# Kernel optimization log

Hardware: AMD Instinct MI355X
Metric: run time of the kernel (lower is better)

The kernel has to match this reference:

```python
import jax, jax.numpy as jnp
import numpy as np

IN_FEATS = 128
OUT_FEATS = 128
ASSIGN_DIM = 256
BATCH_SIZE = 8
N = 12288
E = 196608
CPG = ASSIGN_DIM // BATCH_SIZE  # clusters per graph (block width of the mask)


def setup_inputs() -> dict:
    key = jax.random.key(0)
    ks = jax.random.split(key, 6)
    x = jax.random.normal(ks[0], (N, IN_FEATS), dtype=jnp.float32)
    edge_index = jax.random.randint(ks[1], (2, E), 0, N, dtype=jnp.int32)
    batch = jnp.sort(jax.random.randint(ks[2], (N,), 0, BATCH_SIZE, dtype=jnp.int32))
    s = 1.0 / np.sqrt(2 * IN_FEATS)
    W_embd = jax.random.uniform(ks[3], (2 * IN_FEATS, OUT_FEATS), minval=-s, maxval=s, dtype=jnp.float32)
    b_embd = jnp.zeros((OUT_FEATS,), jnp.float32)
    W_pool = jax.random.uniform(ks[4], (2 * IN_FEATS, ASSIGN_DIM), minval=-s, maxval=s, dtype=jnp.float32)
    b_pool = jnp.zeros((ASSIGN_DIM,), jnp.float32)
    return dict(x=x, edge_index=edge_index, batch=batch,
                W_embd=W_embd, b_embd=b_embd, W_pool=W_pool, b_pool=b_pool)


def _sage_conv(x, src, dst, W, b):
    # GraphSAGE mean aggregator, concat([self, agg]) @ W + b, row L2-normalize.
    agg = jax.ops.segment_sum(x[src], dst, num_segments=N)                 # [N, F]
    deg = jax.ops.segment_sum(jnp.ones((E,), x.dtype), dst, num_segments=N)
    agg = agg / jnp.maximum(deg, 1.0)[:, None]
    h = jnp.concatenate([x, agg], axis=-1) @ W + b
    return h / jnp.maximum(jnp.linalg.norm(h, axis=-1, keepdims=True), 1e-12)


def _masked_softmax_nonme(m, mask):
    # memory_efficient=False branch of masked_softmax
    r = jax.nn.softmax(m * mask, axis=-1)
    r = r * mask
    return r / (r.sum(axis=-1, keepdims=True) + 1e-13)


def reference(x, edge_index, batch, W_embd, b_embd, W_pool, b_pool):
    src, dst = edge_index[0], edge_index[1]
    embed = _sage_conv(x, src, dst, W_embd, b_embd)    # [N, out_feats]
    pooled = _sage_conv(x, src, dst, W_pool, b_pool)   # [N, assign_dim]

    # block-diagonal mask: node i sees the assign columns of its own graph
    col_graph = jnp.arange(ASSIGN_DIM, dtype=batch.dtype) // CPG
    mask = (batch[:, None] == col_graph[None, :]).astype(pooled.dtype)  # [N, assign_dim]

    result = _masked_softmax_nonme(pooled, mask)        # [N, assign_dim]
    h = result.T @ embed                                # [assign_dim, out_feats]

    # adjacency coarsening: S^T A S with edge weights = 1 (duplicates sum)
    Ar = jax.ops.segment_sum(result[dst], src, num_segments=N)  # A @ result
    adj_new = result.T @ Ar                              # [assign_dim, assign_dim]

    # link prediction loss: ||A_dense - S S^T||_F / N^2 (dense NxN, as original)
    A_dense = jnp.zeros((N, N), result.dtype).at[src, dst].add(1.0)
    adj_loss = jnp.linalg.norm(A_dense - result @ result.T) / (N ** 2)

    # entropy loss over Categorical(probs=mask): uniform over each block
    p = mask / mask.sum(axis=-1, keepdims=True)
    ent = -jnp.sum(jnp.where(p > 0, p * jnp.log(jnp.where(p > 0, p, 1.0)), 0.0), axis=-1)
    entropy_loss = ent.sum()

    return adj_new, h, adj_loss, entropy_loss
```

## Files before the change

### kernel.cpp

```cpp
#include <hip/hip_runtime.h>
#include <math.h>

#define NN 12288
#define EE 196608
#define FIN 128
#define AD 256
#define NG 8
#define ACH 32
#define GCH 16
#define BCAP 128
#define APITCH 8256
#define HPITCH 4160
#define GPITCH 1088

using short8 = __attribute__((ext_vector_type(8))) short;
using floatx4 = __attribute__((ext_vector_type(4))) float;

__device__ __forceinline__ unsigned short f2bf(float f) {
  union { float f; unsigned u; } v; v.f = f;
  unsigned r = v.u + 0x7FFFu + ((v.u >> 16) & 1u);
  return (unsigned short)(r >> 16);
}


__global__ __launch_bounds__(256) void k_setup(const float* __restrict__ We, const float* __restrict__ be,
    const float* __restrict__ Wp, const float* __restrict__ bp, const int* __restrict__ batch,
    unsigned* cnt_dst, unsigned* cnt_src, double* acc, unsigned* done,
    unsigned short* __restrict__ WTb, float* __restrict__ bcat, int* __restrict__ gstart) {
  unsigned i = blockIdx.x * 256u + threadIdx.x;
  if (i < 384u * 256u) {
    unsigned n = i >> 8, k = i & 255u;
    float v = (n < 128u) ? We[k * 128u + n] : Wp[k * 256u + (n - 128u)];
    WTb[i] = f2bf(v);
  }
  if (i < 384u) bcat[i] = (i < 128u) ? be[i] : bp[i - 128u];
  if (i < NN) { cnt_dst[i] = 0u; cnt_src[i] = 0u; }
  if (i < 3u) acc[i] = 0.0;
  if (i == 3u) *done = 0u;
  if (i <= NG) {
    int g = (int)i, lo = 0, hi = NN;
    while (lo < hi) { int mid = (lo + hi) >> 1; if (batch[mid] < g) lo = mid + 1; else hi = mid; }
    gstart[g] = lo;
  }
}


__global__ __launch_bounds__(256) void k_edgeB(const int* __restrict__ src, const int* __restrict__ dst,
    const int* __restrict__ batch,
    unsigned* cnt_dst, unsigned* cnt_src, int* __restrict__ bdst, int* __restrict__ bsrc) {
  unsigned e = blockIdx.x * 256u + threadIdx.x;
  if (e >= EE) return;
  int s = src[e], d = dst[e];
  unsigned p = atomicAdd(&cnt_dst[d], 1u);
  if (p < BCAP) bdst[(size_t)d * BCAP + p] = s;
  int gd = batch[d];
  unsigned q = atomicAdd(&cnt_src[s], 1u);
  if (q < BCAP) bsrc[(size_t)s * BCAP + q] = (gd << 14) | d;
}


__global__ __launch_bounds__(256) void k_dupagg(const float* __restrict__ x,
    const unsigned* __restrict__ cnt_dst, const int* __restrict__ bdst,
    unsigned short* __restrict__ Zb, unsigned* __restrict__ dup_part) {
  int node = blockIdx.x * 4 + (threadIdx.x >> 6);
  int lane = threadIdx.x & 63;
  unsigned deg = cnt_dst[node];
  unsigned m = deg < BCAP ? deg : BCAP;
  const int* bk = bdst + (size_t)node * BCAP;
  unsigned cnt = 0;
  for (unsigned i0 = 0; i0 < m; i0 += 64) {
    int si = (i0 + lane < m) ? bk[i0 + lane] : -1;
    for (unsigned j = 0; j < m; j++) {
      int sj = bk[j];
      cnt += (si == sj) ? 1u : 0u;
    }
  }
#pragma unroll
  for (int o = 32; o >= 1; o >>= 1) cnt += __shfl_xor(cnt, o, 64);
  if (lane == 0) dup_part[node] = cnt;
  const float2* x2 = (const float2*)x;
  float ax = 0.f, ay = 0.f;
  for (unsigned k = 0; k < m; k++) {
    int s = bk[k];
    float2 v = x2[(size_t)s * 64 + lane];
    ax += v.x; ay += v.y;
  }
  float inv = 1.f / fmaxf((float)deg, 1.f);
  float2 sv = x2[(size_t)node * 64 + lane];
  ushort2* Zb2 = (ushort2*)Zb;
  ushort2 a; a.x = f2bf(sv.x); a.y = f2bf(sv.y);
  ushort2 mm; mm.x = f2bf(ax * inv); mm.y = f2bf(ay * inv);
  Zb2[(size_t)node * 128 + lane] = a;
  Zb2[(size_t)node * 128 + 64 + lane] = mm;
}


__global__ __launch_bounds__(256) void k_gemmnorm(const unsigned short* __restrict__ Zb,
    const unsigned short* __restrict__ WTb, const float* __restrict__ bcat,
    const int* __restrict__ batch, float* __restrict__ embed, float* __restrict__ Rc) {
  __shared__ unsigned short Bl[24 * 512];
  __shared__ unsigned short Al[4 * 512];
  int t = threadIdx.x;
  int gm = blockIdx.x * 64;
  int w = t >> 6, l = t & 63;

  floatx4 acc[24] = {};

  for (int kc = 0; kc < 8; kc++) {
    __syncthreads();
#pragma unroll
    for (int i = 0; i < 7; i++) {
      int p = t + i * 256;
      if (p < 1536) {
        int n = p >> 2, quad = p & 3;
        uint4 v = *(const uint4*)&WTb[(size_t)n * 256 + kc * 32 + quad * 8];
        *(uint4*)&Bl[(n >> 4) * 512 + ((n & 15) + 16 * quad) * 8] = v;
      } else {
        int p2 = p - 1536;
        int m = p2 >> 2, quad = p2 & 3;
        uint4 v = *(const uint4*)&Zb[(size_t)(gm + m) * 256 + kc * 32 + quad * 8];
        *(uint4*)&Al[(m >> 4) * 512 + ((m & 15) + 16 * quad) * 8] = v;
      }
    }
    __syncthreads();
    short8 a = *(const short8*)&Al[w * 512 + l * 8];
#pragma unroll
    for (int tt = 0; tt < 24; tt++) {
      short8 b = *(const short8*)&Bl[tt * 512 + l * 8];
      acc[tt] = __builtin_amdgcn_mfma_f32_16x16x32_bf16(a, b, acc[tt], 0, 0, 0);
    }
  }

  int col16 = l & 15, quad = l >> 4;
#pragma unroll
  for (int tt = 0; tt < 24; tt++) {
    float b = bcat[tt * 16 + col16];
    acc[tt][0] += b; acc[tt][1] += b; acc[tt][2] += b; acc[tt][3] += b;
  }

#pragma unroll
  for (int r = 0; r < 4; r++) {
    int node = gm + w * 16 + quad * 4 + r;
    float ss = 0.f;
#pragma unroll
    for (int tt = 0; tt < 8; tt++) { float v = acc[tt][r]; ss += v * v; }
#pragma unroll
    for (int o = 8; o >= 1; o >>= 1) ss += __shfl_xor(ss, o, 64);
    float inv = 1.f / fmaxf(sqrtf(ss), 1e-12f);
#pragma unroll
    for (int tt = 0; tt < 8; tt++)
      embed[(size_t)node * 128 + tt * 16 + col16] = acc[tt][r] * inv;
    float ss2 = 0.f;
#pragma unroll
    for (int tt = 8; tt < 24; tt++) { float v = acc[tt][r]; ss2 += v * v; }
#pragma unroll
    for (int o = 8; o >= 1; o >>= 1) ss2 += __shfl_xor(ss2, o, 64);
    float inv2 = 1.f / fmaxf(sqrtf(ss2), 1e-12f);
    int g = batch[node];
    float v0 = 0.f, v1 = 0.f;
#pragma unroll
    for (int tg = 0; tg < 8; tg++) {
      bool sel = (tg == g);
      v0 = sel ? acc[8 + 2 * tg][r] : v0;
      v1 = sel ? acc[9 + 2 * tg][r] : v1;
    }
    v0 *= inv2; v1 *= inv2;
    float mx = fmaxf(v0, v1);
#pragma unroll
    for (int o = 8; o >= 1; o >>= 1) mx = fmaxf(mx, __shfl_xor(mx, o, 64));
    float e0 = expf(v0 - mx), e1 = expf(v1 - mx);
    float sm = e0 + e1;
#pragma unroll
    for (int o = 8; o >= 1; o >>= 1) sm += __shfl_xor(sm, o, 64);
    float rr = 1.f / sm;
    Rc[(size_t)node * 32 + col16] = e0 * rr;
    Rc[(size_t)node * 32 + 16 + col16] = e1 * rr;
  }
}


__global__ __launch_bounds__(256) void k_ar(const float* __restrict__ Rc,
    const unsigned* __restrict__ cnt_src, const int* __restrict__ bsrc,
    float* __restrict__ Ar) {
  int node = blockIdx.x * 4 + (threadIdx.x >> 6);
  int lane = threadIdx.x & 63;
  int lg = lane >> 3, li = lane & 7;
  unsigned deg = cnt_src[node];
  unsigned m = deg < BCAP ? deg : BCAP;
  const int* bk = bsrc + (size_t)node * BCAP;
  float4 acc = {0.f, 0.f, 0.f, 0.f};
  const float4* R4 = (const float4*)Rc;
  for (unsigned k = 0; k < m; k++) {
    int packed = bk[k];
    int d = packed & 16383, g = packed >> 14;
    if (lg == g) {
      float4 r = R4[(size_t)d * 8 + li];
      acc.x += r.x; acc.y += r.y; acc.z += r.z; acc.w += r.w;
    }
  }
  ((float4*)Ar)[(size_t)node * 64 + lane] = acc;
}


__global__ __launch_bounds__(256) void k_big3(const float* __restrict__ Rc,
    const float* __restrict__ embed, const float* __restrict__ Ar, const int* __restrict__ gstart,
    float* __restrict__ part_h, float* __restrict__ part_adj, float* __restrict__ Gpart) {
  int role = blockIdx.z;
  int g = blockIdx.x, ch = blockIdx.y;
  if (role == 2 && ch >= GCH) return;
  int s0 = gstart[g], e0 = gstart[g + 1];
  int nch = (role == 2) ? GCH : ACH;
  int per = (e0 - s0 + nch - 1) / nch;
  int i0 = s0 + ch * per;
  int i1 = i0 + per; if (i1 > e0) i1 = e0;
  int t = threadIdx.x;
  __shared__ float rcs[128][32];

  if (role == 0) {
    int f4 = t & 31, c1g = t >> 5;
    float4 acc[4] = {};
    const float4* E4 = (const float4*)embed;
    for (int ib = i0; ib < i1; ib += 64) {
      int cnt = i1 - ib; if (cnt > 64) cnt = 64;
      __syncthreads();
      const float4* s4 = (const float4*)(Rc + (size_t)ib * 32);
      for (int idx = t; idx < cnt * 8; idx += 256) ((float4*)rcs)[idx] = s4[idx];
      __syncthreads();
      for (int n = 0; n < cnt; n++) {
        float4 e4 = E4[(size_t)(ib + n) * 32 + f4];
        float4 r = *(const float4*)&rcs[n][c1g * 4];
        float rv[4] = {r.x, r.y, r.z, r.w};
#pragma unroll
        for (int j = 0; j < 4; j++) {
          acc[j].x += rv[j] * e4.x; acc[j].y += rv[j] * e4.y;
          acc[j].z += rv[j] * e4.z; acc[j].w += rv[j] * e4.w;
        }
      }
    }
    float* p = part_h + (size_t)(g * ACH + ch) * HPITCH;
#pragma unroll
    for (int j = 0; j < 4; j++)
      *(float4*)&p[(c1g * 4 + j) * 128 + f4 * 4] = acc[j];
  } else if (role == 1) {
    int c2q = t & 63, c1g = t >> 6;
    float4 acc[8] = {};
    const float4* Ar4 = (const float4*)Ar;
    for (int ib = i0; ib < i1; ib += 64) {
      int cnt = i1 - ib; if (cnt > 64) cnt = 64;
      __syncthreads();
      const float4* s4 = (const float4*)(Rc + (size_t)ib * 32);
      for (int idx = t; idx < cnt * 8; idx += 256) ((float4*)rcs)[idx] = s4[idx];
      __syncthreads();
      for (int n = 0; n < cnt; n++) {
        float4 a4 = Ar4[(size_t)(ib + n) * 64 + c2q];
        float4 r0 = *(const float4*)&rcs[n][c1g * 8];
        float4 r1 = *(const float4*)&rcs[n][c1g * 8 + 4];
        float rv[8] = {r0.x, r0.y, r0.z, r0.w, r1.x, r1.y, r1.z, r1.w};
#pragma unroll
        for (int j = 0; j < 8; j++) {
          acc[j].x += rv[j] * a4.x; acc[j].y += rv[j] * a4.y;
          acc[j].z += rv[j] * a4.z; acc[j].w += rv[j] * a4.w;
        }
      }
    }
    float* p = part_adj + (size_t)(g * ACH + ch) * APITCH;
#pragma unroll
    for (int j = 0; j < 8; j++)
      *(float4*)&p[(c1g * 8 + j) * 256 + c2q * 4] = acc[j];
  } else {
    int c2q = t & 7, c1 = t >> 3;
    float4 acc = {};
    for (int ib = i0; ib < i1; ib += 128) {
      int cnt = i1 - ib; if (cnt > 128) cnt = 128;
      __syncthreads();
      const float4* s4 = (const float4*)(Rc + (size_t)ib * 32);
      for (int idx = t; idx < cnt * 8; idx += 256) ((float4*)rcs)[idx] = s4[idx];
      __syncthreads();
      for (int n = 0; n < cnt; n++) {
        float4 r2 = *(const float4*)&rcs[n][c2q * 4];
        float r1 = rcs[n][c1];
        acc.x += r1 * r2.x; acc.y += r1 * r2.y; acc.z += r1 * r2.z; acc.w += r1 * r2.w;
      }
    }
    *(float4*)&Gpart[(size_t)(g * GCH + ch) * GPITCH + c1 * 32 + c2q * 4] = acc;
  }
}


__global__ __launch_bounds__(256) void k_red3(const float* __restrict__ part_adj,
    const float* __restrict__ part_h, const float* __restrict__ Gpart,
    const unsigned* __restrict__ dup_part,
    float* __restrict__ outa, float* __restrict__ outh,
    double* __restrict__ acc, unsigned* __restrict__ done, float* __restrict__ out) {
  int b = blockIdx.x, t = threadIdx.x;
  int lane = t & 63;
  if (b < 256) {
    int i = b * 256 + t;
    int g = i >> 13, off = i & 8191;
    const float* base = part_adj + (size_t)g * ACH * APITCH + off;
    float s = 0.f;
#pragma unroll
    for (int ch = 0; ch < ACH; ch++) s += base[(size_t)ch * APITCH];
    outa[i] = s;
    if (t == b) atomicAdd(&acc[0], (double)s);
  } else if (b < 384) {
    int j = (b - 256) * 256 + t;
    int g = j >> 12, off = j & 4095;
    const float* base = part_h + (size_t)g * ACH * HPITCH + off;
    float s = 0.f;
#pragma unroll
    for (int ch = 0; ch < ACH; ch++) s += base[(size_t)ch * HPITCH];
    outh[j] = s;
  } else if (b < 416) {
    int j = (b - 384) * 256 + t;
    int g = j >> 10, off = j & 1023;
    const float* base = Gpart + (size_t)g * GCH * GPITCH + off;
    float s = 0.f;
#pragma unroll
    for (int ch = 0; ch < GCH; ch++) s += base[(size_t)ch * GPITCH];
    double g2 = (double)s * (double)s;
#pragma unroll
    for (int o = 32; o >= 1; o >>= 1) g2 += __shfl_xor(g2, o, 64);
    if (lane == 0) atomicAdd(&acc[1], g2);
  } else {
    int j = (b - 416) * 256 + t;
    double a2 = (double)dup_part[j];
#pragma unroll
    for (int o = 32; o >= 1; o >>= 1) a2 += __shfl_xor(a2, o, 64);
    if (lane == 0) atomicAdd(&acc[2], a2);
  }
  __syncthreads();
  if (t == 0) {
    unsigned prev = atomicAdd(done, 1u);
    if (prev == gridDim.x - 1) {
      double trf = atomicAdd(&acc[0], 0.0);
      double g2f = atomicAdd(&acc[1], 0.0);
      double a2f = atomicAdd(&acc[2], 0.0);
      double val = a2f - 2.0 * trf + g2f;
      if (val < 0.0) val = 0.0;
      out[98304] = (float)(sqrt(val) / ((double)NN * (double)NN));
      out[98305] = (float)((double)NN * log(32.0));
    }
  }
}


extern "C" void kernel_launch(void* const* d_in, const int* in_sizes, int n_in,
                              void* d_out, int out_size, void* d_ws, size_t ws_size,
                              hipStream_t stream) {
  const float* x = (const float*)d_in[0];
  const int* ei = (const int*)d_in[1];
  const int* src = ei;
  const int* dst = ei + EE;
  const int* batch = (const int*)d_in[2];
  const float* Wemb = (const float*)d_in[3];
  const float* bemb = (const float*)d_in[4];
  const float* Wpool = (const float*)d_in[5];
  const float* bpool = (const float*)d_in[6];
  float* out = (float*)d_out;

  char* w = (char*)d_ws;
  size_t off = 0;
  auto A = [&](size_t bytes) -> char* {
    char* p = w + off;
    off += (bytes + 255) & ~(size_t)255;
    return p;
  };
  unsigned* cnt_dst = (unsigned*)A(NN * 4);
  unsigned* cnt_src = (unsigned*)A(NN * 4);
  int* bdst = (int*)A((size_t)NN * BCAP * 4);
  int* bsrc = (int*)A((size_t)NN * BCAP * 4);
  int* gstart = (int*)A(64);
  unsigned* dup_part = (unsigned*)A(NN * 4);
  double* acc = (double*)A(3 * 8);
  unsigned* done = (unsigned*)A(4);
  unsigned short* Zb = (unsigned short*)A((size_t)NN * 256 * 2);
  float* embed = (float*)A((size_t)NN * FIN * 4);
  float* Rc = (float*)A((size_t)NN * 32 * 4);
  float* Ar = (float*)A((size_t)NN * AD * 4);
  unsigned short* WTb = (unsigned short*)A(384 * 256 * 2);
  float* bcat = (float*)A(384 * 4);
  float* part_h = (float*)A((size_t)8 * ACH * HPITCH * 4);
  float* part_adj = (float*)A((size_t)8 * ACH * APITCH * 4);
  float* Gpart = (float*)A((size_t)8 * GCH * GPITCH * 4);
  (void)ws_size; (void)in_sizes; (void)n_in; (void)out_size;

  k_setup<<<dim3(384), dim3(256), 0, stream>>>(Wemb, bemb, Wpool, bpool, batch,
      cnt_dst, cnt_src, acc, done, WTb, bcat, gstart);
  k_edgeB<<<dim3(EE / 256), dim3(256), 0, stream>>>(src, dst, batch, cnt_dst, cnt_src, bdst, bsrc);
  k_dupagg<<<dim3(NN / 4), dim3(256), 0, stream>>>(x, cnt_dst, bdst, Zb, dup_part);
  k_gemmnorm<<<dim3(NN / 64), dim3(256), 0, stream>>>(Zb, WTb, bcat, batch, embed, Rc);
  k_ar<<<dim3(NN / 4), dim3(256), 0, stream>>>(Rc, cnt_src, bsrc, Ar);
  k_big3<<<dim3(8, ACH, 3), dim3(256), 0, stream>>>(Rc, embed, Ar, gstart, part_h, part_adj, Gpart);
  k_red3<<<dim3(464), dim3(256), 0, stream>>>(part_adj, part_h, Gpart, dup_part,
      out, out + 65536, acc, done, out);
}
```

Before: 196.5 us.

## Process eight nodes per wavefront in k_ar and halve adjacency chunk count

The A@S aggregation kernel now maps one node to each group of 8 lanes, so a wave handles 8 nodes instead of 1. Every lane loads the neighbour's 32-wide compact row and adds it into one of 8 per-graph register accumulators chosen by predicate. Lanes no longer sit idle waiting on a single node's edge loop. The cost is more registers, divergence across the 8 nodes' degrees (looped to the wave's maximum), and wider scattered stores. The chunk count for the big reduction kernel drops from 32 to 16, so its role-2 early exit is removed and fewer partials are produced.

```diff
diff --git a/kernel.cpp b/kernel.cpp
--- a/kernel.cpp
+++ b/kernel.cpp
@@ -6,7 +6,7 @@
 #define FIN 128
 #define AD 256
 #define NG 8
-#define ACH 32
+#define ACH 16
 #define GCH 16
 #define BCAP 128
 #define APITCH 8256
@@ -182,23 +182,38 @@
 __global__ __launch_bounds__(256) void k_ar(const float* __restrict__ Rc,
     const unsigned* __restrict__ cnt_src, const int* __restrict__ bsrc,
     float* __restrict__ Ar) {
-  int node = blockIdx.x * 4 + (threadIdx.x >> 6);
-  int lane = threadIdx.x & 63;
-  int lg = lane >> 3, li = lane & 7;
+  int w = threadIdx.x >> 6, l = threadIdx.x & 63;
+  int sub = l >> 3, li = l & 7;
+  int node = blockIdx.x * 32 + w * 8 + sub;
   unsigned deg = cnt_src[node];
   unsigned m = deg < BCAP ? deg : BCAP;
   const int* bk = bsrc + (size_t)node * BCAP;
-  float4 acc = {0.f, 0.f, 0.f, 0.f};
   const float4* R4 = (const float4*)Rc;
-  for (unsigned k = 0; k < m; k++) {
-    int packed = bk[k];
-    int d = packed & 16383, g = packed >> 14;
-    if (lg == g) {
+  float4 acc[8] = {};
+  unsigned mmax = m;
+#pragma unroll
+  for (int o = 8; o < 64; o <<= 1) {
+    unsigned v = (unsigned)__shfl_xor((int)mmax, o, 64);
+    mmax = mmax > v ? mmax : v;
+  }
+  for (unsigned k = 0; k < mmax; k++) {
+    if (k < m) {
+      int packed = bk[k];
+      int d = packed & 16383, g = packed >> 14;
       float4 r = R4[(size_t)d * 8 + li];
-      acc.x += r.x; acc.y += r.y; acc.z += r.z; acc.w += r.w;
-    }
-  }
-  ((float4*)Ar)[(size_t)node * 64 + lane] = acc;
+#pragma unroll
+      for (int gg = 0; gg < 8; gg++) {
+        bool s = (gg == g);
+        acc[gg].x += s ? r.x : 0.f;
+        acc[gg].y += s ? r.y : 0.f;
+        acc[gg].z += s ? r.z : 0.f;
+        acc[gg].w += s ? r.w : 0.f;
+      }
+    }
+  }
+#pragma unroll
+  for (int gg = 0; gg < 8; gg++)
+    *(float4*)&Ar[(size_t)node * 256 + gg * 32 + li * 4] = acc[gg];
 }
 
 
@@ -207,7 +222,6 @@
     float* __restrict__ part_h, float* __restrict__ part_adj, float* __restrict__ Gpart) {
   int role = blockIdx.z;
   int g = blockIdx.x, ch = blockIdx.y;
-  if (role == 2 && ch >= GCH) return;
   int s0 = gstart[g], e0 = gstart[g + 1];
   int nch = (role == 2) ? GCH : ACH;
   int per = (e0 - s0 + nch - 1) / nch;
@@ -390,7 +404,7 @@
   k_edgeB<<<dim3(EE / 256), dim3(256), 0, stream>>>(src, dst, batch, cnt_dst, cnt_src, bdst, bsrc);
   k_dupagg<<<dim3(NN / 4), dim3(256), 0, stream>>>(x, cnt_dst, bdst, Zb, dup_part);
   k_gemmnorm<<<dim3(NN / 64), dim3(256), 0, stream>>>(Zb, WTb, bcat, batch, embed, Rc);
-  k_ar<<<dim3(NN / 4), dim3(256), 0, stream>>>(Rc, cnt_src, bsrc, Ar);
+  k_ar<<<dim3(NN / 32), dim3(256), 0, stream>>>(Rc, cnt_src, bsrc, Ar);
   k_big3<<<dim3(8, ACH, 3), dim3(256), 0, stream>>>(Rc, embed, Ar, gstart, part_h, part_adj, Gpart);
   k_red3<<<dim3(464), dim3(256), 0, stream>>>(part_adj, part_h, Gpart, dup_part,
       out, out + 65536, acc, done, out);
```

Result: slower. 201.5 us (+2.6%).
